# Optimization experiments

Measured on AMD Instinct MI355X. Metric: run time of the kernel, lower is better.

Reference implementation:

```python
import jax, jax.numpy as jnp
import numpy as np

B, N, E = 32, 2048, 4096
D_IN, C, H = 256, 64, 4          # node_hidden_size, gnn_hidden_size, num_heads
SLOPE = 0.2                       # PyG GATConv default negative_slope


def gat_conv(x, src, dst, W, att_src, att_dst, bias):
    """One PyG-style GATConv (concat=True, add_self_loops=True) on a single graph.
    x: [N, Din]; src/dst: [E] int; W: [Din, H*C]; att_*: [H, C]; bias: [H*C]."""
    n = x.shape[0]
    h = (x @ W).reshape(n, H, C)                       # [N,H,C]
    a_src = jnp.einsum('nhc,hc->nh', h, att_src)       # [N,H]
    a_dst = jnp.einsum('nhc,hc->nh', h, att_dst)
    loop = jnp.arange(n, dtype=src.dtype)              # self loops
    s = jnp.concatenate([src, loop])
    d = jnp.concatenate([dst, loop])
    e = jax.nn.leaky_relu(a_src[s] + a_dst[d], SLOPE)  # [E+N,H]
    # segment softmax over incoming edges of each target node
    m = jax.ops.segment_max(e, d, num_segments=n)
    ex = jnp.exp(e - m[d])
    denom = jax.ops.segment_sum(ex, d, num_segments=n)
    alpha = ex / (denom[d] + 1e-16)                    # [E+N,H]
    out = jax.ops.segment_sum(alpha[:, :, None] * h[s], d, num_segments=n)  # [N,H,C]
    return out.reshape(n, H * C) + bias


def setup_inputs() -> dict:
    key = jax.random.key(0)
    ks = jax.random.split(key, 12)
    g = lambda k, shp, fan: jax.random.normal(k, shp, jnp.float32) * (1.0 / np.sqrt(fan))
    return {
        'node_embeddings': jax.random.normal(ks[0], (B, N, D_IN), jnp.float32),
        'src_index': jax.random.randint(ks[1], (B, E), 0, N, jnp.int32),
        'tgt_index': jax.random.randint(ks[2], (B, E), 0, N, jnp.int32),
        'W1': g(ks[3], (D_IN, H * C), D_IN),
        'att_src1': g(ks[4], (H, C), C),
        'att_dst1': g(ks[5], (H, C), C),
        'bias1': jnp.zeros((H * C,), jnp.float32),
        'W2': g(ks[6], (H * C, H * C), H * C),
        'att_src2': g(ks[7], (H, C), C),
        'att_dst2': g(ks[8], (H, C), C),
        'bias2': jnp.zeros((H * C,), jnp.float32),
    }


def reference(node_embeddings, src_index, tgt_index, W1, att_src1, att_dst1, bias1,
              W2, att_src2, att_dst2, bias2):
    def per_graph(x, s, d):
        m = gat_conv(x, s, d, W1, att_src1, att_dst1, bias1)
        m = jax.nn.elu(m)                              # dropout = identity (eval)
        m = gat_conv(m, s, d, W2, att_src2, att_dst2, bias2)
        return m
    return jax.vmap(per_graph)(node_embeddings, src_index, tgt_index)  # [B,N,H*C]
```

## Files before the change

kernel.cpp:

```cpp
#include <hip/hip_runtime.h>
#include <hip/hip_bf16.h>
#include <cstdint>

#define BB 32
#define NN 2048
#define EE 4096
#define HH 4
#define CC 64
#define DD 256
#define MM (BB*NN)

typedef __attribute__((ext_vector_type(8))) short bf16x8;
typedef __attribute__((ext_vector_type(8))) unsigned short u16x8;
typedef __attribute__((ext_vector_type(4))) float f32x4;

__device__ __forceinline__ float b2f(__hip_bfloat16 x){ return __bfloat162float(x); }
__device__ __forceinline__ float u2f(unsigned short u){ return __uint_as_float((unsigned)u << 16); }
__device__ __forceinline__ unsigned short f2u(float f){
  __hip_bfloat16 h = __float2bfloat16(f);
  return *(unsigned short*)&h;
}
__device__ __forceinline__ float ldany(const void* p, int isf, size_t i){
  return isf ? ((const float*)p)[i] : b2f(((const __hip_bfloat16*)p)[i]);
}
__device__ __forceinline__ void gld_lds16(const void* g, void* l){
  __builtin_amdgcn_global_load_lds((const __attribute__((address_space(1))) uint32_t*)g,
                                   (__attribute__((address_space(3))) uint32_t*)l, 16, 0, 0);
}

__global__ void detect_kernel(const unsigned* __restrict__ w, int* __restrict__ flag){
  __shared__ int cnt;
  if(threadIdx.x == 0) cnt = 0;
  __syncthreads();
  int c = 0;
  #pragma unroll
  for(int i = 0; i < 4; ++i){
    unsigned v = w[threadIdx.x*4 + i];
    unsigned elo = (v >> 7) & 0xFFu;
    if(elo >= 100u && elo <= 150u) ++c;
  }
  atomicAdd(&cnt, c);
  __syncthreads();
  if(threadIdx.x == 0) *flag = (cnt < 128) ? 1 : 0;
}

__global__ __launch_bounds__(256) void prep_kernel(const void* __restrict__ W1,
    const void* __restrict__ W2, __hip_bfloat16* __restrict__ W1t,
    __hip_bfloat16* __restrict__ W2t,
    const void* s0, const void* s1, const void* s2, const void* s3,
    const void* s4, const void* s5, float* __restrict__ attf,
    int* __restrict__ degc, const int* __restrict__ flag)
{
  int isf = *flag;
  int bid = blockIdx.x, t = threadIdx.x;
  if(bid < 512){
    const void* W = (bid < 256) ? W1 : W2;
    __hip_bfloat16* WT = (bid < 256) ? W1t : W2t;
    int i = (bid & 255)*256 + t;
    WT[i] = __float2bfloat16(ldany(W, isf, (size_t)(i & 255)*256 + (i >> 8)));
  } else if(bid < 518){
    int i = (bid - 512)*256 + t;
    int seg = i >> 8, off = i & 255;
    const void* s = seg==0?s0 : seg==1?s1 : seg==2?s2 : seg==3?s3 : seg==4?s4 : s5;
    attf[i] = ldany(s, isf, off);
  } else {
    int i = (bid - 518)*256 + t;
    int4 z = {0,0,0,0};
    *((int4*)degc + i) = z;
  }
}

__global__ __launch_bounds__(256) void convX_kernel(const float* __restrict__ src,
    unsigned short* __restrict__ dst, const int* __restrict__ flag){
  if(!*flag) return;
  int blk  = blockIdx.x;
  int vblk = (blk & 7)*2048 + (blk >> 3);
  size_t i = ((size_t)vblk*256 + threadIdx.x)*4;
  float4 v = *(const float4*)(src + i);
  ushort4 o = { f2u(v.x), f2u(v.y), f2u(v.z), f2u(v.w) };
  *(ushort4*)(dst + i) = o;
}

template<int DYNA>
__global__ __launch_bounds__(256, 3) void mfma_gemm(const __hip_bfloat16* __restrict__ A0,
    const __hip_bfloat16* __restrict__ A1, const __hip_bfloat16* __restrict__ BT,
    __hip_bfloat16* __restrict__ C,
    const float* __restrict__ attS, const float* __restrict__ attD,
    float* __restrict__ aS, float* __restrict__ aD, const int* __restrict__ flag)
{
  __shared__ __align__(16) short lds[24576];
  const int tid  = threadIdx.x;
  const int w    = tid >> 6, lane = tid & 63;
  const int dd   = blockIdx.x;
  const int xcd  = dd & 7, slot = dd >> 3;
  const int rb   = xcd*64 + (slot >> 1), cb = slot & 1;
  const int row0 = rb*128, col0 = cb*128;
  const int wr   = (w & 1)*64, wc = (w >> 1)*64;
  const int fm   = lane & 15, quad = lane >> 4;
  const short* Ab = (const short*)A0;
  if(DYNA && *flag) Ab = (const short*)A1;
  const short* Bb = (const short*)BT;

  const int jof   = lane >> 3;
  const int rpar  = (lane >> 2) & 1;
  const int lslot = lane & 3;

  const int headI = (col0 + wc) >> 6;
  float ws_[4], wd_[4];
  #pragma unroll
  for(int j = 0; j < 4; ++j){
    ws_[j] = attS[headI*CC + j*16 + fm];
    wd_[j] = attD[headI*CC + j*16 + fm];
  }

  f32x4 acc[4][4] = {};

  auto stage = [&](int t, short* buf){
    #pragma unroll
    for(int c = 0; c < 2; ++c){
      int j = w*16 + c*8 + jof;
      int s = lslot ^ (j & 3);
      const short* ga = Ab + (size_t)(row0 + 2*j + rpar)*DD + t*32 + s*8;
      gld_lds16(ga, buf + (w*16 + c*8)*64);
    }
    #pragma unroll
    for(int c = 0; c < 2; ++c){
      int j = w*16 + c*8 + jof;
      int s = lslot ^ (j & 3);
      const short* gb = Bb + (size_t)(col0 + 2*j + rpar)*DD + t*32 + s*8;
      gld_lds16(gb, buf + 4096 + (w*16 + c*8)*64);
    }
  };
  auto compute = [&](const short* buf){
    const short* lA = buf;
    const short* lB = buf + 4096;
    bf16x8 af[4], bfv[4];
    #pragma unroll
    for(int i = 0; i < 4; ++i){
      int m = wr + i*16 + fm;
      af[i]  = *(const bf16x8*)&lA[(m >> 1)*64 + (((m & 1)*4 + (quad ^ ((m >> 1) & 3)))*8)];
      int n = wc + i*16 + fm;
      bfv[i] = *(const bf16x8*)&lB[(n >> 1)*64 + (((n & 1)*4 + (quad ^ ((n >> 1) & 3)))*8)];
    }
    #pragma unroll
    for(int i = 0; i < 4; ++i)
      #pragma unroll
      for(int j = 0; j < 4; ++j)
        acc[i][j] = __builtin_amdgcn_mfma_f32_16x16x32_bf16(af[i], bfv[j], acc[i][j], 0, 0, 0);
  };

  stage(0, lds);
  stage(1, lds + 8192);
  asm volatile("s_waitcnt vmcnt(4)" ::: "memory");
  __builtin_amdgcn_sched_barrier(0);
  __builtin_amdgcn_s_barrier();
  #pragma unroll
  for(int t = 0; t < 8; ++t){
    if(t < 6) stage(t + 2, lds + ((t + 2) % 3)*8192);
    compute(lds + (t % 3)*8192);
    if(t < 6) asm volatile("s_waitcnt vmcnt(4)" ::: "memory");
    else      asm volatile("s_waitcnt vmcnt(0)" ::: "memory");
    __builtin_amdgcn_sched_barrier(0);
    asm volatile("s_waitcnt lgkmcnt(0)" ::: "memory");
    __builtin_amdgcn_sched_barrier(0);
    __builtin_amdgcn_s_barrier();
  }

  #pragma unroll
  for(int i = 0; i < 4; ++i){
    #pragma unroll
    for(int r = 0; r < 4; ++r){
      float s = 0.f, dv = 0.f;
      #pragma unroll
      for(int j = 0; j < 4; ++j){
        float v = acc[i][j][r];
        s  += v * ws_[j];
        dv += v * wd_[j];
      }
      #pragma unroll
      for(int m = 1; m <= 8; m <<= 1){
        s  += __shfl_xor(s,  m);
        dv += __shfl_xor(dv, m);
      }
      if(fm == i*4 + r){
        int row = row0 + wr + i*16 + quad*4 + r;
        aS[(size_t)row*HH + headI] = s;
        aD[(size_t)row*HH + headI] = dv;
      }
    }
  }

  #pragma unroll
  for(int i = 0; i < 4; ++i)
    #pragma unroll
    for(int j = 0; j < 4; ++j)
      #pragma unroll
      for(int r = 0; r < 4; ++r){
        int rl = wr + i*16 + quad*4 + r;
        int cl = wc + j*16 + fm;
        lds[rl*128 + (cl ^ ((rl & 12) << 2))] = (short)f2u(acc[i][j][r]);
      }
  __syncthreads();
  const int rr = tid >> 4, cc = (tid & 15)*8;
  #pragma unroll
  for(int p = 0; p < 8; ++p){
    int rl = p*16 + rr;
    u16x8 v = *(const u16x8*)&lds[rl*128 + (cc ^ ((rl & 12) << 2))];
    *(u16x8*)((unsigned short*)C + (size_t)(row0 + rl)*DD + col0 + cc) = v;
  }
}

__global__ __launch_bounds__(256) void deg_kernel(const int* __restrict__ dst, int* __restrict__ degc)
{
  int idx = blockIdx.x*256 + threadIdx.x;
  if(idx >= BB*EE) return;
  int b = idx >> 12;
  atomicAdd(&degc[b*NN + dst[idx]], 1);
}

__global__ __launch_bounds__(256) void scan_kernel(int* __restrict__ degc, int* __restrict__ row_ptr)
{
  __shared__ int part[256];
  int b = blockIdx.x, t = threadIdx.x;
  int loc[8], s = 0;
  #pragma unroll
  for(int i = 0; i < 8; ++i){ loc[i] = s; s += degc[b*NN + t*8 + i]; }
  part[t] = s;
  __syncthreads();
  if(t == 0){
    int run = 0;
    for(int i = 0; i < 256; ++i){ int tmp = part[i]; part[i] = run; run += tmp; }
  }
  __syncthreads();
  int base = b*EE + part[t];
  #pragma unroll
  for(int i = 0; i < 8; ++i){
    int v = base + loc[i];
    row_ptr[b*(NN+1) + t*8 + i] = v;
    degc   [b*NN     + t*8 + i] = v;
  }
  if(t == 255) row_ptr[b*(NN+1) + NN] = base + s;
}

__global__ __launch_bounds__(256) void scatter_kernel(const int* __restrict__ src,
    const int* __restrict__ dst, int* __restrict__ cursor, unsigned short* __restrict__ srcList)
{
  int idx = blockIdx.x*256 + threadIdx.x;
  if(idx >= BB*EE) return;
  int b = idx >> 12;
  int pos = atomicAdd(&cursor[b*NN + dst[idx]], 1);
  srcList[pos] = (unsigned short)src[idx];
}

template<int LAYER>
__global__ __launch_bounds__(256) void gather_kernel(const __hip_bfloat16* __restrict__ H,
    const float* __restrict__ a_src, const float* __restrict__ a_dst,
    const int* __restrict__ row_ptr, const unsigned short* __restrict__ srcList,
    const float* __restrict__ bias, void* __restrict__ outp,
    const int* __restrict__ flag)
{
  int blk  = blockIdx.x;
  int vblk = (blk & 7)*2048 + (blk >> 3);
  int wid  = vblk*4 + (int)(threadIdx.x >> 6);
  int lane = threadIdx.x & 63;
  int b = wid >> 11, d = wid & (NN-1);
  int head = lane >> 4;
  int start = row_ptr[b*(NN+1) + d];
  int end   = row_ptr[b*(NN+1) + d + 1];
  const unsigned short* Hu = (const unsigned short*)H;

  float adv = a_dst[wid*HH + head];
  float sv  = a_src[wid*HH + head] + adv;
  sv = sv > 0.f ? sv : 0.2f*sv;
  float exs = __expf(sv);

  ushort4 hv = *(const ushort4*)(Hu + (size_t)wid*DD + lane*4);
  f32x4 acc;
  acc.x = exs*u2f(hv.x); acc.y = exs*u2f(hv.y); acc.z = exs*u2f(hv.z); acc.w = exs*u2f(hv.w);
  float den = exs;

  int e = start;
  float ax = 0.f; ushort4 hw = {0,0,0,0};
  if(e < end){
    int s = srcList[e];
    ax = a_src[(b*NN + s)*HH + head];
    hw = *(const ushort4*)(Hu + (size_t)(b*NN + s)*DD + lane*4);
  }
  while(e < end){
    float axn = 0.f; ushort4 hwn = {0,0,0,0};
    if(e + 1 < end){
      int sn = srcList[e+1];
      axn = a_src[(b*NN + sn)*HH + head];
      hwn = *(const ushort4*)(Hu + (size_t)(b*NN + sn)*DD + lane*4);
    }
    float v = ax + adv;
    v = v > 0.f ? v : 0.2f*v;
    float ex = __expf(v);
    acc.x += ex*u2f(hw.x); acc.y += ex*u2f(hw.y); acc.z += ex*u2f(hw.z); acc.w += ex*u2f(hw.w);
    den += ex;
    ax = axn; hw = hwn; ++e;
  }
  float inv = 1.f / (den + 1e-16f);
  float4 bs = *(const float4*)(bias + lane*4);
  float o0 = acc.x*inv + bs.x, o1 = acc.y*inv + bs.y;
  float o2 = acc.z*inv + bs.z, o3 = acc.w*inv + bs.w;
  size_t oi = (size_t)wid*DD + lane*4;
  if(LAYER == 1){
    o0 = o0 > 0.f ? o0 : expm1f(o0);
    o1 = o1 > 0.f ? o1 : expm1f(o1);
    o2 = o2 > 0.f ? o2 : expm1f(o2);
    o3 = o3 > 0.f ? o3 : expm1f(o3);
    ushort4 ov = { f2u(o0), f2u(o1), f2u(o2), f2u(o3) };
    *(ushort4*)((unsigned short*)outp + oi) = ov;
  } else {
    if(*flag){
      float4 ov = { o0, o1, o2, o3 };
      *(float4*)((float*)outp + oi) = ov;
    } else {
      ushort4 ov = { f2u(o0), f2u(o1), f2u(o2), f2u(o3) };
      *(ushort4*)((unsigned short*)outp + oi) = ov;
    }
  }
}

extern "C" void kernel_launch(void* const* d_in, const int* in_sizes, int n_in,
                              void* d_out, int out_size, void* d_ws, size_t ws_size,
                              hipStream_t stream)
{
  const void* x_in = d_in[0];
  const int*  srcI = (const int*)d_in[1];
  const int*  dstI = (const int*)d_in[2];
  const void* W1   = d_in[3];
  const void* as1  = d_in[4];
  const void* ad1  = d_in[5];
  const void* b1   = d_in[6];
  const void* W2   = d_in[7];
  const void* as2  = d_in[8];
  const void* ad2  = d_in[9];
  const void* b2   = d_in[10];

  char* ws = (char*)d_ws;
  __hip_bfloat16* R1  = (__hip_bfloat16*)ws; ws += (size_t)MM*DD*2;
  __hip_bfloat16* R2  = (__hip_bfloat16*)ws; ws += (size_t)MM*DD*2;
  float* a_src = (float*)ws; ws += (size_t)MM*HH*4;
  float* a_dst = (float*)ws; ws += (size_t)MM*HH*4;
  __hip_bfloat16* W1t = (__hip_bfloat16*)ws; ws += (size_t)DD*DD*2;
  __hip_bfloat16* W2t = (__hip_bfloat16*)ws; ws += (size_t)DD*DD*2;
  float* attf = (float*)ws; ws += 1536*4;
  int*   degc = (int*)ws;   ws += (size_t)BB*NN*4;
  int*   rowp = (int*)ws;   ws += (size_t)BB*(NN+1)*4;
  unsigned short* srcL = (unsigned short*)ws; ws += (size_t)BB*EE*2;
  int*   flag = (int*)ws;   ws += 8;

  const int gemmBlocks   = (MM/128)*(DD/128);
  const int edgeBlocks   = (BB*EE)/256;
  const int gatherBlocks = (MM*64)/256;

  detect_kernel<<<1, 64, 0, stream>>>((const unsigned*)x_in, flag);
  prep_kernel<<<582, 256, 0, stream>>>(W1, W2, W1t, W2t,
                                       as1, ad1, b1, as2, ad2, b2, attf, degc, flag);
  convX_kernel<<<(int)(((size_t)MM*DD)/1024), 256, 0, stream>>>((const float*)x_in,
                                       (unsigned short*)R1, flag);

  deg_kernel    <<<edgeBlocks, 256, 0, stream>>>(dstI, degc);
  scan_kernel   <<<BB,         256, 0, stream>>>(degc, rowp);
  scatter_kernel<<<edgeBlocks, 256, 0, stream>>>(srcI, dstI, degc, srcL);

  mfma_gemm<1><<<gemmBlocks, 256, 0, stream>>>((const __hip_bfloat16*)x_in, R1, W1t, R2,
                                               attf + 0, attf + 256, a_src, a_dst, flag);
  gather_kernel<1><<<gatherBlocks, 256, 0, stream>>>(R2, a_src, a_dst, rowp, srcL,
                                                     attf + 512, R1, flag);
  mfma_gemm<0><<<gemmBlocks, 256, 0, stream>>>(R1, nullptr, W2t, R2,
                                               attf + 768, attf + 1024, a_src, a_dst, flag);
  gather_kernel<2><<<gatherBlocks, 256, 0, stream>>>(R2, a_src, a_dst, rowp, srcL,
                                                     attf + 1280, d_out, flag);
}
```

Baseline: 245.8 us.

## Load GEMM operand fragments directly from global into registers, bypassing LDS staging

Replaces the LDS-staged pipeline (global_load_lds into a triple-buffered swizzled tile plus barriers) with direct per-lane global loads of MFMA fragments into a three-deep register ring, and drops occupancy to 2 blocks per CU. The goal is to remove barrier and LDS round-trip overhead. In exchange, every wave re-reads A and B fragments from global or L2 with no sharing through LDS, and register pressure rises. The lds array is still declared, resized, presumably for the epilogue.

```diff
diff --git a/kernel.cpp b/kernel.cpp
--- a/kernel.cpp
+++ b/kernel.cpp
@@ -22,10 +22,6 @@
 }
 __device__ __forceinline__ float ldany(const void* p, int isf, size_t i){
   return isf ? ((const float*)p)[i] : b2f(((const __hip_bfloat16*)p)[i]);
-}
-__device__ __forceinline__ void gld_lds16(const void* g, void* l){
-  __builtin_amdgcn_global_load_lds((const __attribute__((address_space(1))) uint32_t*)g,
-                                   (__attribute__((address_space(3))) uint32_t*)l, 16, 0, 0);
 }
 
 __global__ void detect_kernel(const unsigned* __restrict__ w, int* __restrict__ flag){
@@ -82,13 +78,13 @@
 }
 
 template<int DYNA>
-__global__ __launch_bounds__(256, 3) void mfma_gemm(const __hip_bfloat16* __restrict__ A0,
+__global__ __launch_bounds__(256, 2) void mfma_gemm(const __hip_bfloat16* __restrict__ A0,
     const __hip_bfloat16* __restrict__ A1, const __hip_bfloat16* __restrict__ BT,
     __hip_bfloat16* __restrict__ C,
     const float* __restrict__ attS, const float* __restrict__ attD,
     float* __restrict__ aS, float* __restrict__ aD, const int* __restrict__ flag)
 {
-  __shared__ __align__(16) short lds[24576];
+  __shared__ __align__(16) short lds[128*128];
   const int tid  = threadIdx.x;
   const int w    = tid >> 6, lane = tid & 63;
   const int dd   = blockIdx.x;
@@ -101,71 +97,40 @@
   if(DYNA && *flag) Ab = (const short*)A1;
   const short* Bb = (const short*)BT;
 
-  const int jof   = lane >> 3;
-  const int rpar  = (lane >> 2) & 1;
-  const int lslot = lane & 3;
-
-  const int headI = (col0 + wc) >> 6;
-  float ws_[4], wd_[4];
-  #pragma unroll
-  for(int j = 0; j < 4; ++j){
-    ws_[j] = attS[headI*CC + j*16 + fm];
-    wd_[j] = attD[headI*CC + j*16 + fm];
-  }
+  const short* pa = Ab + (size_t)(row0 + wr + fm)*DD + quad*8;
+  const short* pb = Bb + (size_t)(col0 + wc + fm)*DD + quad*8;
 
   f32x4 acc[4][4] = {};
-
-  auto stage = [&](int t, short* buf){
+  bf16x8 fa[3][4], fb[3][4];
+
+  auto loadc = [&](int t, int b){
     #pragma unroll
-    for(int c = 0; c < 2; ++c){
-      int j = w*16 + c*8 + jof;
-      int s = lslot ^ (j & 3);
-      const short* ga = Ab + (size_t)(row0 + 2*j + rpar)*DD + t*32 + s*8;
-      gld_lds16(ga, buf + (w*16 + c*8)*64);
-    }
-    #pragma unroll
-    for(int c = 0; c < 2; ++c){
-      int j = w*16 + c*8 + jof;
-      int s = lslot ^ (j & 3);
-      const short* gb = Bb + (size_t)(col0 + 2*j + rpar)*DD + t*32 + s*8;
-      gld_lds16(gb, buf + 4096 + (w*16 + c*8)*64);
+    for(int i = 0; i < 4; ++i){
+      fa[b][i] = *(const bf16x8*)(pa + (size_t)i*16*DD + t*32);
+      fb[b][i] = *(const bf16x8*)(pb + (size_t)i*16*DD + t*32);
     }
   };
-  auto compute = [&](const short* buf){
-    const short* lA = buf;
-    const short* lB = buf + 4096;
-    bf16x8 af[4], bfv[4];
-    #pragma unroll
-    for(int i = 0; i < 4; ++i){
-      int m = wr + i*16 + fm;
-      af[i]  = *(const bf16x8*)&lA[(m >> 1)*64 + (((m & 1)*4 + (quad ^ ((m >> 1) & 3)))*8)];
-      int n = wc + i*16 + fm;
-      bfv[i] = *(const bf16x8*)&lB[(n >> 1)*64 + (((n & 1)*4 + (quad ^ ((n >> 1) & 3)))*8)];
-    }
+
+  loadc(0, 0);
+  loadc(1, 1);
+  #pragma unroll
+  for(int t = 0; t < 8; ++t){
+    if(t < 6) loadc(t + 2, (t + 2) % 3);
+    const int b = t % 3;
     #pragma unroll
     for(int i = 0; i < 4; ++i)
       #pragma unroll
       for(int j = 0; j < 4; ++j)
-        acc[i][j] = __builtin_amdgcn_mfma_f32_16x16x32_bf16(af[i], bfv[j], acc[i][j], 0, 0, 0);
-  };
-
-  stage(0, lds);
-  stage(1, lds + 8192);
-  asm volatile("s_waitcnt vmcnt(4)" ::: "memory");
-  __builtin_amdgcn_sched_barrier(0);
-  __builtin_amdgcn_s_barrier();
-  #pragma unroll
-  for(int t = 0; t < 8; ++t){
-    if(t < 6) stage(t + 2, lds + ((t + 2) % 3)*8192);
-    compute(lds + (t % 3)*8192);
-    if(t < 6) asm volatile("s_waitcnt vmcnt(4)" ::: "memory");
-    else      asm volatile("s_waitcnt vmcnt(0)" ::: "memory");
-    __builtin_amdgcn_sched_barrier(0);
-    asm volatile("s_waitcnt lgkmcnt(0)" ::: "memory");
-    __builtin_amdgcn_sched_barrier(0);
-    __builtin_amdgcn_s_barrier();
-  }
-
+        acc[i][j] = __builtin_amdgcn_mfma_f32_16x16x32_bf16(fa[b][i], fb[b][j], acc[i][j], 0, 0, 0);
+  }
+
+  const int headI = (col0 + wc) >> 6;
+  float ws_[4], wd_[4];
+  #pragma unroll
+  for(int j = 0; j < 4; ++j){
+    ws_[j] = attS[headI*CC + j*16 + fm];
+    wd_[j] = attD[headI*CC + j*16 + fm];
+  }
   #pragma unroll
   for(int i = 0; i < 4; ++i){
     #pragma unroll
```

New measurement: 286.7 us. 1.17x slower.
